# Kernel optimization log

Hardware: AMD Instinct MI355X
Metric: run time of the kernel (lower is better)

## Reference

```python
import jax, jax.numpy as jnp
import numpy as np

NUM_LAYERS = 3


def setup_inputs() -> dict:
    key = jax.random.key(0)
    k1, k2 = jax.random.split(key)
    N = 200000          # num_users + num_items
    D = 64              # latent_dim
    E = 4000000         # number of directed edges
    edge_index = jax.random.randint(k1, (2, E), 0, N, dtype=jnp.int64)
    emb_weight = 0.1 * jax.random.normal(k2, (N, D), dtype=jnp.float32)  # nn.init.normal_(std=0.1)
    return {"edge_index": edge_index, "emb_weight": emb_weight}


def reference(edge_index, emb_weight):
    N, D = emb_weight.shape
    src, dst = edge_index[0], edge_index[1]
    # gcn_norm (no self loops), as used by LGConv
    deg = jax.ops.segment_sum(jnp.ones_like(src, dtype=emb_weight.dtype), dst, num_segments=N)
    dinv = jnp.where(deg > 0, jax.lax.rsqrt(jnp.maximum(deg, 1.0)), 0.0)
    norm = dinv[src] * dinv[dst]            # [E]
    emb0 = emb_weight
    emb = emb0
    acc = emb0                              # running sum over layer embeddings
    for _ in range(NUM_LAYERS):
        msgs = norm[:, None] * emb[src]     # [E, D] irregular gather
        emb = jax.ops.segment_sum(msgs, dst, num_segments=N)  # scatter-add aggregate
        acc = acc + emb
    out = acc / (NUM_LAYERS + 1)            # mean over stacked layer embeddings
    return (emb0, out)
```

## Files before the change

kernel.cpp:

```cpp
#include <hip/hip_runtime.h>
#include <hip/hip_fp16.h>

#define DIM 64
#define BNODE_SHIFT 8
#define BNODE (1 << BNODE_SHIFT)
#define MAXNB 1024
#define BCAP_SHIFT 13
#define BCAP (1 << BCAP_SHIFT)
#define BIN_MAXCHUNK 16384

__device__ inline __half2 as_h2(unsigned int u) {
    union { unsigned int u; __half2 h; } x; x.u = u; return x.h;
}
__device__ inline unsigned int as_u32(__half2 h) {
    union { unsigned int u; __half2 h; } x; x.h = h; return x.u;
}

__global__ void init_cursor_kernel(int* __restrict__ cursor, int NB) {
    int b = blockIdx.x * blockDim.x + threadIdx.x;
    if (b < NB) cursor[b] = b << BCAP_SHIFT;
}

__global__ void zero_rows_kernel(unsigned int* __restrict__ SX,
                                 unsigned int* __restrict__ SY, int N) {
    int t = threadIdx.x;
    SX[(size_t)N * (DIM / 2) + t] = 0u;
    SY[(size_t)N * (DIM / 2) + t] = 0u;
}

__global__ void __launch_bounds__(512) bin3_kernel(
        const int* __restrict__ src, const int* __restrict__ dst,
        int* __restrict__ cursor, unsigned int* __restrict__ packed,
        int E, int NB, int CHUNK) {
    __shared__ int lhist[MAXNB];
    __shared__ int lbase[MAXNB];
    __shared__ unsigned short srank[BIN_MAXCHUNK];
    const int t = threadIdx.x;
    for (int i = t; i < MAXNB; i += 512) lhist[i] = 0;
    __syncthreads();
    const long long beg = (long long)blockIdx.x * CHUNK;
    long long lim = beg + CHUNK;
    if (lim > E) lim = E;
    for (long long idx = beg + t; idx < lim; idx += 512) {
        int d = dst[idx];
        int c = atomicAdd(&lhist[d >> BNODE_SHIFT], 1);
        srank[(int)(idx - beg)] = (unsigned short)c;
    }
    __syncthreads();
    for (int b = t; b < NB; b += 512) {
        int c = lhist[b];
        lbase[b] = c ? atomicAdd(&cursor[b], c) : 0;
    }
    __syncthreads();
    for (long long idx = beg + t; idx < lim; idx += 512) {
        int d = dst[idx];
        int b = d >> BNODE_SHIFT;
        int c = srank[(int)(idx - beg)];
        packed[lbase[b] + c] =
            (unsigned int)src[idx] | ((unsigned int)(d & (BNODE - 1)) << 18);
    }
}

__global__ void __launch_bounds__(BNODE) csr3_kernel(
        const int* __restrict__ cursor, const unsigned int* __restrict__ packed,
        int* __restrict__ csr_src, float* __restrict__ dinv,
        int4* __restrict__ desc, int N) {
    __shared__ int hist[BNODE];
    __shared__ int s[BNODE];
    __shared__ int soff[BNODE];
    __shared__ unsigned short rnk[BCAP];
    const int t = threadIdx.x;
    const int b = blockIdx.x;
    const int b0 = b << BCAP_SHIFT;
    const int cnt = cursor[b] - b0;
    hist[t] = 0;
    __syncthreads();
    for (int i = t; i < cnt; i += BNODE) {
        int c = atomicAdd(&hist[packed[b0 + i] >> 18], 1);
        rnk[i] = (unsigned short)c;
    }
    __syncthreads();
    s[t] = hist[t];
    __syncthreads();
    for (int off = 1; off < BNODE; off <<= 1) {
        int v = s[t];
        int a = (t >= off) ? s[t - off] : 0;
        __syncthreads();
        s[t] = v + a;
        __syncthreads();
    }
    const int deg = hist[t];
    const int excl = s[t] - deg;
    soff[t] = excl;
    const int myBeg = b0 + excl;
    const int node = (b << BNODE_SHIFT) + t;
    if (node < N) {
        float fd = (float)deg;
        float di2 = deg > 0 ? 1.0f / fd : 0.0f;
        dinv[node] = deg > 0 ? rsqrtf(fd) : 0.0f;
        desc[node] = make_int4(myBeg, myBeg + deg, deg, __float_as_int(di2));
    }
    __syncthreads();
    for (int i = t; i < cnt; i += BNODE) {
        unsigned int p = packed[b0 + i];
        csr_src[b0 + soff[p >> 18] + rnk[i]] = (int)(p & 0x3FFFFu);
    }
}

__global__ void conv0_kernel(const float* __restrict__ emb0, const float* __restrict__ dinv,
                             float* __restrict__ out_emb0, unsigned int* __restrict__ S0,
                             int n4) {
    int i = blockIdx.x * blockDim.x + threadIdx.x;
    if (i >= n4) return;
    float4 v = ((const float4*)emb0)[i];
    ((float4*)out_emb0)[i] = v;
    float w = dinv[i >> 4];
    uint2 o;
    o.x = as_u32(__float22half2_rn(make_float2(w * v.x, w * v.y)));
    o.y = as_u32(__float22half2_rn(make_float2(w * v.z, w * v.w)));
    ((uint2*)S0)[i] = o;
}

template<bool LAST>
__global__ void gather_kernel(const int4* __restrict__ desc,
                              const int* __restrict__ csr_src,
                              const unsigned int* __restrict__ S_in,
                              unsigned int* __restrict__ S_out,
                              const unsigned int* __restrict__ S1,
                              const float* __restrict__ emb0,
                              float* __restrict__ acc,
                              int N) {
    const int node = (blockIdx.x * blockDim.x + threadIdx.x) >> 6;
    if (node >= N) return;
    const int lane = threadIdx.x & 63;
    const int eg = lane >> 3;
    const int q  = lane & 7;
    const int4 d = desc[node];
    const int end = d.y;
    __half2 a0 = as_h2(0u), a1 = as_h2(0u), a2 = as_h2(0u), a3 = as_h2(0u);
    for (int i0 = d.x + eg; i0 < end; i0 += 32) {
        int r0 = csr_src[i0];
        int r1 = csr_src[i0 + 8];
        int r2 = csr_src[i0 + 16];
        int r3 = csr_src[i0 + 24];
        int s0 = r0;
        int s1 = (i0 + 8  < end) ? r1 : N;
        int s2 = (i0 + 16 < end) ? r2 : N;
        int s3 = (i0 + 24 < end) ? r3 : N;
        uint4 g0 = *(const uint4*)(S_in + (size_t)s0 * (DIM / 2) + q * 4);
        uint4 g1 = *(const uint4*)(S_in + (size_t)s1 * (DIM / 2) + q * 4);
        uint4 g2 = *(const uint4*)(S_in + (size_t)s2 * (DIM / 2) + q * 4);
        uint4 g3 = *(const uint4*)(S_in + (size_t)s3 * (DIM / 2) + q * 4);
        a0 = __hadd2(a0, as_h2(g0.x)); a1 = __hadd2(a1, as_h2(g0.y));
        a2 = __hadd2(a2, as_h2(g0.z)); a3 = __hadd2(a3, as_h2(g0.w));
        a0 = __hadd2(a0, as_h2(g1.x)); a1 = __hadd2(a1, as_h2(g1.y));
        a2 = __hadd2(a2, as_h2(g1.z)); a3 = __hadd2(a3, as_h2(g1.w));
        a0 = __hadd2(a0, as_h2(g2.x)); a1 = __hadd2(a1, as_h2(g2.y));
        a2 = __hadd2(a2, as_h2(g2.z)); a3 = __hadd2(a3, as_h2(g2.w));
        a0 = __hadd2(a0, as_h2(g3.x)); a1 = __hadd2(a1, as_h2(g3.y));
        a2 = __hadd2(a2, as_h2(g3.z)); a3 = __hadd2(a3, as_h2(g3.w));
    }
    #pragma unroll
    for (int m = 8; m < 64; m <<= 1) {
        a0 = __hadd2(a0, as_h2(__shfl_xor(as_u32(a0), m, 64)));
        a1 = __hadd2(a1, as_h2(__shfl_xor(as_u32(a1), m, 64)));
        a2 = __hadd2(a2, as_h2(__shfl_xor(as_u32(a2), m, 64)));
        a3 = __hadd2(a3, as_h2(__shfl_xor(as_u32(a3), m, 64)));
    }
    if (lane >= 8) return;
    const float di2 = __int_as_float(d.w);
    float2 f0 = __half22float2(a0);
    float2 f1 = __half22float2(a1);
    float2 f2 = __half22float2(a2);
    float2 f3 = __half22float2(a3);
    if (!LAST) {
        uint4 o;
        o.x = as_u32(__float22half2_rn(make_float2(di2 * f0.x, di2 * f0.y)));
        o.y = as_u32(__float22half2_rn(make_float2(di2 * f1.x, di2 * f1.y)));
        o.z = as_u32(__float22half2_rn(make_float2(di2 * f2.x, di2 * f2.y)));
        o.w = as_u32(__float22half2_rn(make_float2(di2 * f3.x, di2 * f3.y)));
        *(uint4*)(S_out + (size_t)node * (DIM / 2) + lane * 4) = o;
    } else {
        float rs = di2 > 0.f ? rsqrtf(di2) : 0.f;
        float dv = sqrtf(di2);
        uint4 u1 = *(const uint4*)(S1   + (size_t)node * (DIM / 2) + lane * 4);
        uint4 u2 = *(const uint4*)(S_in + (size_t)node * (DIM / 2) + lane * 4);
        float2 b0 = __half22float2(as_h2(u1.x)), c0 = __half22float2(as_h2(u2.x));
        float2 b1 = __half22float2(as_h2(u1.y)), c1 = __half22float2(as_h2(u2.y));
        float2 b2 = __half22float2(as_h2(u1.z)), c2 = __half22float2(as_h2(u2.z));
        float2 b3 = __half22float2(as_h2(u1.w)), c3 = __half22float2(as_h2(u2.w));
        const float* e = emb0 + (size_t)node * DIM + lane * 8;
        float4 e0 = *(const float4*)(e);
        float4 e1 = *(const float4*)(e + 4);
        float4 o0, o1;
        o0.x = 0.25f * (e0.x + rs * (b0.x + c0.x) + dv * f0.x);
        o0.y = 0.25f * (e0.y + rs * (b0.y + c0.y) + dv * f0.y);
        o0.z = 0.25f * (e0.z + rs * (b1.x + c1.x) + dv * f1.x);
        o0.w = 0.25f * (e0.w + rs * (b1.y + c1.y) + dv * f1.y);
        o1.x = 0.25f * (e1.x + rs * (b2.x + c2.x) + dv * f2.x);
        o1.y = 0.25f * (e1.y + rs * (b2.y + c2.y) + dv * f2.y);
        o1.z = 0.25f * (e1.z + rs * (b3.x + c3.x) + dv * f3.x);
        o1.w = 0.25f * (e1.w + rs * (b3.y + c3.y) + dv * f3.y);
        float* ap = acc + (size_t)node * DIM + lane * 8;
        *(float4*)(ap) = o0;
        *(float4*)(ap + 4) = o1;
    }
}

static inline size_t align256(size_t x) { return (x + 255) & ~(size_t)255; }

extern "C" void kernel_launch(void* const* d_in, const int* in_sizes, int n_in,
                              void* d_out, int out_size, void* d_ws, size_t ws_size,
                              hipStream_t stream) {
    const int*   edge = (const int*)d_in[0];
    const float* emb0 = (const float*)d_in[1];
    const int E = in_sizes[0] / 2;
    const int N = in_sizes[1] / DIM;
    const int* src = edge;
    const int* dst = edge + E;
    const int NB = (N + BNODE - 1) >> BNODE_SHIFT;

    int bin_blocks = 256;
    int chunk = (E + bin_blocks - 1) / bin_blocks;
    if (chunk > BIN_MAXCHUNK) {
        bin_blocks = (E + BIN_MAXCHUNK - 1) / BIN_MAXCHUNK;
        chunk = (E + bin_blocks - 1) / bin_blocks;
    }

    char* ws = (char*)d_ws;
    int* cursor        = (int*)ws;  ws += align256((size_t)(MAXNB + 1) * sizeof(int));
    float* dinv        = (float*)ws; ws += align256((size_t)N * sizeof(float));
    int4* desc         = (int4*)ws; ws += align256((size_t)N * sizeof(int4));
    unsigned int* packed = (unsigned int*)ws; ws += align256((size_t)NB * BCAP * sizeof(int));
    int* csr_src       = (int*)ws;  ws += align256(((size_t)NB * BCAP + 64) * sizeof(int));
    unsigned int* SX   = (unsigned int*)ws; ws += align256((size_t)(N + 1) * (DIM / 2) * sizeof(unsigned int));
    unsigned int* SY   = (unsigned int*)ws; ws += align256((size_t)(N + 1) * (DIM / 2) * sizeof(unsigned int));

    float* out_emb0 = (float*)d_out;
    float* acc      = out_emb0 + (size_t)N * DIM;

    const int n4 = N * DIM / 4;

    init_cursor_kernel<<<(NB + 255) / 256, 256, 0, stream>>>(cursor, NB);
    zero_rows_kernel<<<1, 32, 0, stream>>>(SX, SY, N);
    bin3_kernel<<<bin_blocks, 512, 0, stream>>>(src, dst, cursor, packed, E, NB, chunk);
    csr3_kernel<<<NB, BNODE, 0, stream>>>(cursor, packed, csr_src, dinv, desc, N);

    conv0_kernel<<<(n4 + 255) / 256, 256, 0, stream>>>(emb0, dinv, out_emb0, SX, n4);

    const long long gthreads = (long long)N * 64;
    const int ggrid = (int)((gthreads + 255) / 256);
    gather_kernel<false><<<ggrid, 256, 0, stream>>>(desc, csr_src, SX, SY, nullptr, nullptr, nullptr, N);
    gather_kernel<false><<<ggrid, 256, 0, stream>>>(desc, csr_src, SY, SX, nullptr, nullptr, nullptr, N);
    gather_kernel<true><<<ggrid, 256, 0, stream>>>(desc, csr_src, SX, nullptr, SY, emb0, acc, N);
}
```

Before: 489.5 us.

## Fuse setup kernels, fold conv0 into CSR build, pre-scale gather indices

Merges the cursor-init and zero-row kernels into one launch and folds the emb0 copy and dinv-scaled half conversion into the CSR construction kernel, using per-block shared dinv values, so the separate dinv buffer and conv0 launch go away. CSR source indices are stored pre-multiplied by the row stride (<<5) to remove a multiply in the gather address math. The gather adds a fast path for nodes with at most 24 neighbours that does a single three-load iteration without the loop. This reduces launch count and a global round trip for dinv, but the CSR kernel now carries extra streaming work per block, and the shifted index relies on N*32 fitting in int.

```diff
diff --git a/kernel.cpp b/kernel.cpp
--- a/kernel.cpp
+++ b/kernel.cpp
@@ -16,16 +16,15 @@
     union { unsigned int u; __half2 h; } x; x.h = h; return x.u;
 }
 
-__global__ void init_cursor_kernel(int* __restrict__ cursor, int NB) {
-    int b = blockIdx.x * blockDim.x + threadIdx.x;
-    if (b < NB) cursor[b] = b << BCAP_SHIFT;
-}
-
-__global__ void zero_rows_kernel(unsigned int* __restrict__ SX,
-                                 unsigned int* __restrict__ SY, int N) {
-    int t = threadIdx.x;
-    SX[(size_t)N * (DIM / 2) + t] = 0u;
-    SY[(size_t)N * (DIM / 2) + t] = 0u;
+__global__ void setup_kernel(int* __restrict__ cursor,
+                             unsigned int* __restrict__ SX,
+                             unsigned int* __restrict__ SY, int NB, int N) {
+    int i = blockIdx.x * blockDim.x + threadIdx.x;
+    if (i < NB) cursor[i] = i << BCAP_SHIFT;
+    if (i < DIM / 2) {
+        SX[(size_t)N * (DIM / 2) + i] = 0u;
+        SY[(size_t)N * (DIM / 2) + i] = 0u;
+    }
 }
 
 __global__ void __launch_bounds__(512) bin3_kernel(
@@ -61,13 +60,15 @@
     }
 }
 
-__global__ void __launch_bounds__(BNODE) csr3_kernel(
+__global__ void __launch_bounds__(BNODE) csr3f_kernel(
         const int* __restrict__ cursor, const unsigned int* __restrict__ packed,
-        int* __restrict__ csr_src, float* __restrict__ dinv,
-        int4* __restrict__ desc, int N) {
+        int* __restrict__ csr_src, int4* __restrict__ desc,
+        const float* __restrict__ emb0, float* __restrict__ out_emb0,
+        unsigned int* __restrict__ SX, int N) {
     __shared__ int hist[BNODE];
     __shared__ int s[BNODE];
     __shared__ int soff[BNODE];
+    __shared__ float sdv[BNODE];
     __shared__ unsigned short rnk[BCAP];
     const int t = threadIdx.x;
     const int b = blockIdx.x;
@@ -94,31 +95,34 @@
     soff[t] = excl;
     const int myBeg = b0 + excl;
     const int node = (b << BNODE_SHIFT) + t;
+    float fd = (float)deg;
+    float dvv = deg > 0 ? rsqrtf(fd) : 0.0f;
+    sdv[t] = dvv;
     if (node < N) {
-        float fd = (float)deg;
         float di2 = deg > 0 ? 1.0f / fd : 0.0f;
-        dinv[node] = deg > 0 ? rsqrtf(fd) : 0.0f;
         desc[node] = make_int4(myBeg, myBeg + deg, deg, __float_as_int(di2));
     }
     __syncthreads();
     for (int i = t; i < cnt; i += BNODE) {
         unsigned int p = packed[b0 + i];
-        csr_src[b0 + soff[p >> 18] + rnk[i]] = (int)(p & 0x3FFFFu);
-    }
-}
-
-__global__ void conv0_kernel(const float* __restrict__ emb0, const float* __restrict__ dinv,
-                             float* __restrict__ out_emb0, unsigned int* __restrict__ S0,
-                             int n4) {
-    int i = blockIdx.x * blockDim.x + threadIdx.x;
-    if (i >= n4) return;
-    float4 v = ((const float4*)emb0)[i];
-    ((float4*)out_emb0)[i] = v;
-    float w = dinv[i >> 4];
-    uint2 o;
-    o.x = as_u32(__float22half2_rn(make_float2(w * v.x, w * v.y)));
-    o.y = as_u32(__float22half2_rn(make_float2(w * v.z, w * v.w)));
-    ((uint2*)S0)[i] = o;
+        csr_src[b0 + soff[p >> 18] + rnk[i]] = (int)((p & 0x3FFFFu) << 5);
+    }
+    const long long base4 = (long long)b * (BNODE * (DIM / 4));
+    const long long lim4 = (long long)N * (DIM / 4);
+    #pragma unroll 4
+    for (int it = 0; it < BNODE * (DIM / 4) / BNODE; ++it) {
+        int idx = it * BNODE + t;
+        long long g = base4 + idx;
+        if (g < lim4) {
+            float4 v = ((const float4*)emb0)[g];
+            ((float4*)out_emb0)[g] = v;
+            float w = sdv[idx >> 4];
+            uint2 o;
+            o.x = as_u32(__float22half2_rn(make_float2(w * v.x, w * v.y)));
+            o.y = as_u32(__float22half2_rn(make_float2(w * v.z, w * v.w)));
+            ((uint2*)SX)[g] = o;
+        }
+    }
 }
 
 template<bool LAST>
@@ -137,28 +141,48 @@
     const int q  = lane & 7;
     const int4 d = desc[node];
     const int end = d.y;
+    const int NS = N << 5;
     __half2 a0 = as_h2(0u), a1 = as_h2(0u), a2 = as_h2(0u), a3 = as_h2(0u);
-    for (int i0 = d.x + eg; i0 < end; i0 += 32) {
+    if (end - d.x <= 24) {
+        int i0 = d.x + eg;
         int r0 = csr_src[i0];
         int r1 = csr_src[i0 + 8];
         int r2 = csr_src[i0 + 16];
-        int r3 = csr_src[i0 + 24];
-        int s0 = r0;
-        int s1 = (i0 + 8  < end) ? r1 : N;
-        int s2 = (i0 + 16 < end) ? r2 : N;
-        int s3 = (i0 + 24 < end) ? r3 : N;
-        uint4 g0 = *(const uint4*)(S_in + (size_t)s0 * (DIM / 2) + q * 4);
-        uint4 g1 = *(const uint4*)(S_in + (size_t)s1 * (DIM / 2) + q * 4);
-        uint4 g2 = *(const uint4*)(S_in + (size_t)s2 * (DIM / 2) + q * 4);
-        uint4 g3 = *(const uint4*)(S_in + (size_t)s3 * (DIM / 2) + q * 4);
+        int s0 = (i0      < end) ? r0 : NS;
+        int s1 = (i0 + 8  < end) ? r1 : NS;
+        int s2 = (i0 + 16 < end) ? r2 : NS;
+        uint4 g0 = *(const uint4*)(S_in + s0 + q * 4);
+        uint4 g1 = *(const uint4*)(S_in + s1 + q * 4);
+        uint4 g2 = *(const uint4*)(S_in + s2 + q * 4);
         a0 = __hadd2(a0, as_h2(g0.x)); a1 = __hadd2(a1, as_h2(g0.y));
         a2 = __hadd2(a2, as_h2(g0.z)); a3 = __hadd2(a3, as_h2(g0.w));
         a0 = __hadd2(a0, as_h2(g1.x)); a1 = __hadd2(a1, as_h2(g1.y));
         a2 = __hadd2(a2, as_h2(g1.z)); a3 = __hadd2(a3, as_h2(g1.w));
         a0 = __hadd2(a0, as_h2(g2.x)); a1 = __hadd2(a1, as_h2(g2.y));
         a2 = __hadd2(a2, as_h2(g2.z)); a3 = __hadd2(a3, as_h2(g2.w));
-        a0 = __hadd2(a0, as_h2(g3.x)); a1 = __hadd2(a1, as_h2(g3.y));
-        a2 = __hadd2(a2, as_h2(g3.z)); a3 = __hadd2(a3, as_h2(g3.w));
+    } else {
+        for (int i0 = d.x + eg; i0 < end; i0 += 32) {
+            int r0 = csr_src[i0];
+            int r1 = csr_src[i0 + 8];
+            int r2 = csr_src[i0 + 16];
+            int r3 = csr_src[i0 + 24];
+            int s0 = r0;
+            int s1 = (i0 + 8  < end) ? r1 : NS;
+            int s2 = (i0 + 16 < end) ? r2 : NS;
+            int s3 = (i0 + 24 < end) ? r3 : NS;
+            uint4 g0 = *(const uint4*)(S_in + s0 + q * 4);
+            uint4 g1 = *(const uint4*)(S_in + s1 + q * 4);
+            uint4 g2 = *(const uint4*)(S_in + s2 + q * 4);
+            uint4 g3 = *(const uint4*)(S_in + s3 + q * 4);
+            a0 = __hadd2(a0, as_h2(g0.x)); a1 = __hadd2(a1, as_h2(g0.y));
+            a2 = __hadd2(a2, as_h2(g0.z)); a3 = __hadd2(a3, as_h2(g0.w));
+            a0 = __hadd2(a0, as_h2(g1.x)); a1 = __hadd2(a1, as_h2(g1.y));
+            a2 = __hadd2(a2, as_h2(g1.z)); a3 = __hadd2(a3, as_h2(g1.w));
+            a0 = __hadd2(a0, as_h2(g2.x)); a1 = __hadd2(a1, as_h2(g2.y));
+            a2 = __hadd2(a2, as_h2(g2.z)); a3 = __hadd2(a3, as_h2(g2.w));
+            a0 = __hadd2(a0, as_h2(g3.x)); a1 = __hadd2(a1, as_h2(g3.y));
+            a2 = __hadd2(a2, as_h2(g3.z)); a3 = __hadd2(a3, as_h2(g3.w));
+        }
     }
     #pragma unroll
     for (int m = 8; m < 64; m <<= 1) {
@@ -229,7 +253,6 @@
 
     char* ws = (char*)d_ws;
     int* cursor        = (int*)ws;  ws += align256((size_t)(MAXNB + 1) * sizeof(int));
-    float* dinv        = (float*)ws; ws += align256((size_t)N * sizeof(float));
     int4* desc         = (int4*)ws; ws += align256((size_t)N * sizeof(int4));
     unsigned int* packed = (unsigned int*)ws; ws += align256((size_t)NB * BCAP * sizeof(int));
     int* csr_src       = (int*)ws;  ws += align256(((size_t)NB * BCAP + 64) * sizeof(int));
@@ -239,14 +262,10 @@
     float* out_emb0 = (float*)d_out;
     float* acc      = out_emb0 + (size_t)N * DIM;
 
-    const int n4 = N * DIM / 4;
-
-    init_cursor_kernel<<<(NB + 255) / 256, 256, 0, stream>>>(cursor, NB);
-    zero_rows_kernel<<<1, 32, 0, stream>>>(SX, SY, N);
+    setup_kernel<<<(NB + 255) / 256, 256, 0, stream>>>(cursor, SX, SY, NB, N);
     bin3_kernel<<<bin_blocks, 512, 0, stream>>>(src, dst, cursor, packed, E, NB, chunk);
-    csr3_kernel<<<NB, BNODE, 0, stream>>>(cursor, packed, csr_src, dinv, desc, N);
-
-    conv0_kernel<<<(n4 + 255) / 256, 256, 0, stream>>>(emb0, dinv, out_emb0, SX, n4);
+    csr3f_kernel<<<NB, BNODE, 0, stream>>>(cursor, packed, csr_src, desc,
+                                           emb0, out_emb0, SX, N);
 
     const long long gthreads = (long long)N * 64;
     const int ggrid = (int)((gthreads + 255) / 256);
```

Result: no change. 497.2 us (+1.6%).
